# Optimization experiments

Measured on AMD Instinct MI355X. Metric: run time of the kernel, lower is better.

## Reference

```python
import jax, jax.numpy as jnp
import numpy as np

PARTITIONS = 8
TWO_PI = 2.0 * np.pi
EPS_COUNT = 0.0001  # added to bin counts to avoid div-by-zero


def setup_inputs() -> dict:
    key = jax.random.key(0)
    k1, k2, k3, k4 = jax.random.split(key, 4)
    B, N, T = 16384, 128, 8
    trajs = jax.random.normal(k1, (B, T, 2), dtype=jnp.float32)
    nei_trajs = jax.random.normal(k2, (B, N, T, 2), dtype=jnp.float32)
    # mark last 32 neighbors as invalid (all-zero trajectories -> masked out)
    nei_trajs = nei_trajs.at[:, N - 32:].set(0.0)
    # TrajEncoding: Dense(dim=3 -> output_units=128) + ReLU
    W_ce = jax.random.normal(k3, (3, 128), dtype=jnp.float32) * (1.0 / np.sqrt(3.0))
    b_ce = jnp.zeros((128,), dtype=jnp.float32)
    return {"trajs": trajs, "nei_trajs": nei_trajs, "W_ce": W_ce, "b_ce": b_ce}


def reference(trajs, nei_trajs, W_ce, b_ce):
    # trajs: [B, T, 2]; nei_trajs: [B, N, T, 2]
    nei_vector = nei_trajs[..., -1, :] - nei_trajs[..., 0, :]      # [B, N, 2]
    nei_pos = nei_trajs[..., -1, :]                                 # [B, N, 2]

    # factors (use_velocity, use_distance, use_direction; rel_velocity=False)
    f_velocity = jnp.linalg.norm(nei_vector, axis=-1)               # [B, N]
    f_distance = jnp.linalg.norm(nei_pos, axis=-1)                  # [B, N]
    f_direction = jnp.arctan2(nei_pos[..., 0], nei_pos[..., 1]) % TWO_PI  # [B, N]

    angle_idx = (f_direction / (TWO_PI / PARTITIONS)).astype(jnp.int32)   # [B, N]
    nei_mask = (jnp.sum(nei_trajs, axis=(-1, -2)) != 0).astype(jnp.int32)  # [B, N]
    angle_idx = angle_idx * nei_mask + (-1) * (1 - nei_mask)

    # one-hot over partitions replaces the python loop: [B, N, P]
    onehot = (angle_idx[..., None] == jnp.arange(PARTITIONS, dtype=jnp.int32)).astype(jnp.float32)
    n = jnp.sum(onehot, axis=1) + EPS_COUNT                         # [B, P]

    feats = jnp.stack([f_velocity, f_distance, f_direction], axis=-1)  # [B, N, 3]
    sums = jnp.einsum('bnf,bnp->bpf', feats, onehot)                # [B, P, 3]
    social_circle = sums / n[..., None]                             # [B, P, 3]

    f_sc = jax.nn.relu(social_circle @ W_ce + b_ce)                 # [B, P, 128]
    return f_sc, social_circle
```

## Files before the change

### kernel.cpp

```cpp
#include <hip/hip_runtime.h>
#include <math.h>

#define NPART 8
#define NN    128

typedef float f32x4 __attribute__((ext_vector_type(4)));

__global__ __launch_bounds__(256) void sc_kernel(
    const float* __restrict__ nei,
    const float* __restrict__ W,
    const float* __restrict__ bce,
    float* __restrict__ fsc,
    float* __restrict__ scout,
    int Btot)
{
    const int tid  = threadIdx.x;
    const int lane = tid & 63;
    const int wv   = tid >> 6;
    const int b    = blockIdx.x * 4 + wv;
    if (b >= Btot) return;

    __shared__ float s_sum[4][NPART * 3];
    __shared__ float s_cnt[4][NPART];
    __shared__ float s_sc[4][NPART * 3];

    const f32x4* src = reinterpret_cast<const f32x4*>(nei) + (size_t)b * (NN * 4);
    f32x4 a0 = __builtin_nontemporal_load(src + lane * 4 + 0);
    f32x4 c0 = __builtin_nontemporal_load(src + lane * 4 + 1);
    f32x4 d0 = __builtin_nontemporal_load(src + lane * 4 + 2);
    f32x4 e0 = __builtin_nontemporal_load(src + lane * 4 + 3);
    f32x4 a1 = __builtin_nontemporal_load(src + 256 + lane * 4 + 0);
    f32x4 c1 = __builtin_nontemporal_load(src + 256 + lane * 4 + 1);
    f32x4 d1 = __builtin_nontemporal_load(src + 256 + lane * 4 + 2);
    f32x4 e1 = __builtin_nontemporal_load(src + 256 + lane * 4 + 3);

    const int c0i = 4 * (lane & 31);
    f32x4 wr0 = *reinterpret_cast<const f32x4*>(W + 0 * NN + c0i);
    f32x4 wr1 = *reinterpret_cast<const f32x4*>(W + 1 * NN + c0i);
    f32x4 wr2 = *reinterpret_cast<const f32x4*>(W + 2 * NN + c0i);
    f32x4 bb  = *reinterpret_cast<const f32x4*>(bce + c0i);

    if (lane < NPART * 3) s_sum[wv][lane] = 0.0f;
    if (lane < NPART)     s_cnt[wv][lane] = 0.0f;
    __builtin_amdgcn_wave_barrier();

    const float TWOPI = 6.2831853071795864769f;
    const float STEP  = (float)(6.283185307179586 / 8.0);

    #pragma unroll
    for (int h = 0; h < 2; ++h) {
        f32x4 a = h ? a1 : a0;
        f32x4 c = h ? c1 : c0;
        f32x4 d = h ? d1 : d0;
        f32x4 e = h ? e1 : e0;

        float total = (((a.x + a.y) + (a.z + a.w)) + ((c.x + c.y) + (c.z + c.w)))
                    + (((d.x + d.y) + (d.z + d.w)) + ((e.x + e.y) + (e.z + e.w)));

        float px = e.z, py = e.w;
        float vx = px - a.x, vy = py - a.y;
        float fvel  = sqrtf(vx * vx + vy * vy);
        float fdist = sqrtf(px * px + py * py);

        float fdir = atan2f(px, py);
        if (fdir < 0.0f) fdir += TWOPI;

        int idx = (int)(fdir / STEP);

        if (total != 0.0f && idx >= 0 && idx < NPART) {
            atomicAdd(&s_sum[wv][idx * 3 + 0], fvel);
            atomicAdd(&s_sum[wv][idx * 3 + 1], fdist);
            atomicAdd(&s_sum[wv][idx * 3 + 2], fdir);
            atomicAdd(&s_cnt[wv][idx], 1.0f);
        }
    }
    __builtin_amdgcn_wave_barrier();

    if (lane < NPART * 3) {
        float v = s_sum[wv][lane] / (s_cnt[wv][lane / 3] + 0.0001f);
        s_sc[wv][lane] = v;
        __builtin_nontemporal_store(v, scout + (size_t)b * (NPART * 3) + lane);
    }
    __builtin_amdgcn_wave_barrier();

    float* o = fsc + (size_t)b * NPART * NN;
    #pragma unroll
    for (int s = 0; s < 4; ++s) {
        int p = 2 * s + (lane >> 5);
        float sv = s_sc[wv][p * 3 + 0];
        float sd = s_sc[wv][p * 3 + 1];
        float sr = s_sc[wv][p * 3 + 2];
        f32x4 acc;
        acc.x = fmaxf(fmaf(sv, wr0.x, fmaf(sd, wr1.x, fmaf(sr, wr2.x, bb.x))), 0.0f);
        acc.y = fmaxf(fmaf(sv, wr0.y, fmaf(sd, wr1.y, fmaf(sr, wr2.y, bb.y))), 0.0f);
        acc.z = fmaxf(fmaf(sv, wr0.z, fmaf(sd, wr1.z, fmaf(sr, wr2.z, bb.z))), 0.0f);
        acc.w = fmaxf(fmaf(sv, wr0.w, fmaf(sd, wr1.w, fmaf(sr, wr2.w, bb.w))), 0.0f);
        __builtin_nontemporal_store(acc, reinterpret_cast<f32x4*>(o + p * NN + c0i));
    }
}

extern "C" void kernel_launch(void* const* d_in, const int* in_sizes, int n_in,
                              void* d_out, int out_size, void* d_ws, size_t ws_size,
                              hipStream_t stream) {
    const float* nei = (const float*)d_in[1];
    const float* W   = (const float*)d_in[2];
    const float* bce = (const float*)d_in[3];

    const int Btot = in_sizes[1] / (NN * 8 * 2);

    float* fsc   = (float*)d_out;
    float* scout = fsc + (size_t)Btot * NPART * NN;

    const int nblk = (Btot + 3) / 4;
    sc_kernel<<<nblk, 256, 0, stream>>>(nei, W, bce, fsc, scout, Btot);
}
```

Before: 51.84 us.

## Use fast polynomial atan2, split LDS histograms per half-wave, drop nontemporal hints

Replaces the library atan2f with a custom minimax polynomial that uses hardware reciprocal and returns the angle directly in [0, 2π). The bin index is now computed by multiplying by a constant instead of dividing. The shared-memory histogram is duplicated per half-wave to cut atomic contention, and the two copies are summed at the end. Nontemporal loads and stores become plain accesses, and the weight loads move after the reduction. This adds a small accuracy risk near bin boundaries and changes how the memory streams are cached.

Measured after the change: 44.30 us. 1.17x faster.

```diff
diff --git a/kernel.cpp b/kernel.cpp
--- a/kernel.cpp
+++ b/kernel.cpp
@@ -5,6 +5,33 @@
 #define NN    128
 
 typedef float f32x4 __attribute__((ext_vector_type(4)));
+
+__device__ __forceinline__ float atan2_2pi(float y, float x) {
+    const float PI_F    = 3.14159265358979f;
+    const float PIO2_F  = 1.57079632679490f;
+    const float PIO4_F  = 0.78539816339745f;
+    const float TWOPI_F = 6.28318530717959f;
+    float ay = fabsf(y), ax = fabsf(x);
+    float mn = fminf(ay, ax), mx = fmaxf(ay, ax);
+    float r  = __builtin_amdgcn_rcpf(mx);
+    float q  = mn * r;
+    q = fmaf(fmaf(-mx, q, mn), r, q);
+    bool  big  = q > 0.41421356237f;
+    float num2 = q - 1.0f, den2 = q + 1.0f;
+    float r2   = __builtin_amdgcn_rcpf(den2);
+    float q2   = num2 * r2;
+    q2 = fmaf(fmaf(-den2, q2, num2), r2, q2);
+    float t = big ? q2 : q;
+    float u = t * t;
+    float p = fmaf(u, 8.05374449538e-2f, -1.38776856032e-1f);
+    p = fmaf(u, p, 1.99777106478e-1f);
+    p = fmaf(u, p, -3.33329491539e-1f);
+    float z0 = fmaf(p * u, t, t);
+    if (big) z0 += PIO4_F;
+    float zq = (ay > ax) ? (PIO2_F - z0) : z0;
+    float z1 = (x < 0.0f) ? (PI_F - zq) : zq;
+    return (y < 0.0f) ? (TWOPI_F - z1) : z1;
+}
 
 __global__ __launch_bounds__(256) void sc_kernel(
     const float* __restrict__ nei,
@@ -17,35 +44,30 @@
     const int tid  = threadIdx.x;
     const int lane = tid & 63;
     const int wv   = tid >> 6;
+    const int hi   = lane >> 5;
     const int b    = blockIdx.x * 4 + wv;
     if (b >= Btot) return;
 
-    __shared__ float s_sum[4][NPART * 3];
-    __shared__ float s_cnt[4][NPART];
+    __shared__ float s_sum[4][2][NPART * 3];
+    __shared__ float s_cnt[4][2][NPART];
     __shared__ float s_sc[4][NPART * 3];
 
     const f32x4* src = reinterpret_cast<const f32x4*>(nei) + (size_t)b * (NN * 4);
-    f32x4 a0 = __builtin_nontemporal_load(src + lane * 4 + 0);
-    f32x4 c0 = __builtin_nontemporal_load(src + lane * 4 + 1);
-    f32x4 d0 = __builtin_nontemporal_load(src + lane * 4 + 2);
-    f32x4 e0 = __builtin_nontemporal_load(src + lane * 4 + 3);
-    f32x4 a1 = __builtin_nontemporal_load(src + 256 + lane * 4 + 0);
-    f32x4 c1 = __builtin_nontemporal_load(src + 256 + lane * 4 + 1);
-    f32x4 d1 = __builtin_nontemporal_load(src + 256 + lane * 4 + 2);
-    f32x4 e1 = __builtin_nontemporal_load(src + 256 + lane * 4 + 3);
+    f32x4 a0 = src[lane * 4 + 0];
+    f32x4 c0 = src[lane * 4 + 1];
+    f32x4 d0 = src[lane * 4 + 2];
+    f32x4 e0 = src[lane * 4 + 3];
+    f32x4 a1 = src[256 + lane * 4 + 0];
+    f32x4 c1 = src[256 + lane * 4 + 1];
+    f32x4 d1 = src[256 + lane * 4 + 2];
+    f32x4 e1 = src[256 + lane * 4 + 3];
 
-    const int c0i = 4 * (lane & 31);
-    f32x4 wr0 = *reinterpret_cast<const f32x4*>(W + 0 * NN + c0i);
-    f32x4 wr1 = *reinterpret_cast<const f32x4*>(W + 1 * NN + c0i);
-    f32x4 wr2 = *reinterpret_cast<const f32x4*>(W + 2 * NN + c0i);
-    f32x4 bb  = *reinterpret_cast<const f32x4*>(bce + c0i);
-
-    if (lane < NPART * 3) s_sum[wv][lane] = 0.0f;
-    if (lane < NPART)     s_cnt[wv][lane] = 0.0f;
+    {
+        int ll = lane & 31;
+        if (ll < NPART * 3) s_sum[wv][hi][ll] = 0.0f;
+        else                s_cnt[wv][hi][ll - NPART * 3] = 0.0f;
+    }
     __builtin_amdgcn_wave_barrier();
-
-    const float TWOPI = 6.2831853071795864769f;
-    const float STEP  = (float)(6.283185307179586 / 8.0);
 
     #pragma unroll
     for (int h = 0; h < 2; ++h) {
@@ -62,31 +84,36 @@
         float fvel  = sqrtf(vx * vx + vy * vy);
         float fdist = sqrtf(px * px + py * py);
 
-        float fdir = atan2f(px, py);
-        if (fdir < 0.0f) fdir += TWOPI;
-
-        int idx = (int)(fdir / STEP);
+        float fdir = atan2_2pi(px, py);
+        int idx = (int)(fdir * 1.27323954474f);
 
         if (total != 0.0f && idx >= 0 && idx < NPART) {
-            atomicAdd(&s_sum[wv][idx * 3 + 0], fvel);
-            atomicAdd(&s_sum[wv][idx * 3 + 1], fdist);
-            atomicAdd(&s_sum[wv][idx * 3 + 2], fdir);
-            atomicAdd(&s_cnt[wv][idx], 1.0f);
+            atomicAdd(&s_sum[wv][hi][idx * 3 + 0], fvel);
+            atomicAdd(&s_sum[wv][hi][idx * 3 + 1], fdist);
+            atomicAdd(&s_sum[wv][hi][idx * 3 + 2], fdir);
+            atomicAdd(&s_cnt[wv][hi][idx], 1.0f);
         }
     }
     __builtin_amdgcn_wave_barrier();
 
     if (lane < NPART * 3) {
-        float v = s_sum[wv][lane] / (s_cnt[wv][lane / 3] + 0.0001f);
+        float v = (s_sum[wv][0][lane] + s_sum[wv][1][lane]) /
+                  (s_cnt[wv][0][lane / 3] + s_cnt[wv][1][lane / 3] + 0.0001f);
         s_sc[wv][lane] = v;
-        __builtin_nontemporal_store(v, scout + (size_t)b * (NPART * 3) + lane);
+        scout[(size_t)b * (NPART * 3) + lane] = v;
     }
     __builtin_amdgcn_wave_barrier();
+
+    const int c0i = 4 * (lane & 31);
+    f32x4 wr0 = *reinterpret_cast<const f32x4*>(W + 0 * NN + c0i);
+    f32x4 wr1 = *reinterpret_cast<const f32x4*>(W + 1 * NN + c0i);
+    f32x4 wr2 = *reinterpret_cast<const f32x4*>(W + 2 * NN + c0i);
+    f32x4 bb  = *reinterpret_cast<const f32x4*>(bce + c0i);
 
     float* o = fsc + (size_t)b * NPART * NN;
     #pragma unroll
     for (int s = 0; s < 4; ++s) {
-        int p = 2 * s + (lane >> 5);
+        int p = 2 * s + hi;
         float sv = s_sc[wv][p * 3 + 0];
         float sd = s_sc[wv][p * 3 + 1];
         float sr = s_sc[wv][p * 3 + 2];
@@ -95,7 +122,7 @@
         acc.y = fmaxf(fmaf(sv, wr0.y, fmaf(sd, wr1.y, fmaf(sr, wr2.y, bb.y))), 0.0f);
         acc.z = fmaxf(fmaf(sv, wr0.z, fmaf(sd, wr1.z, fmaf(sr, wr2.z, bb.z))), 0.0f);
         acc.w = fmaxf(fmaf(sv, wr0.w, fmaf(sd, wr1.w, fmaf(sr, wr2.w, bb.w))), 0.0f);
-        __builtin_nontemporal_store(acc, reinterpret_cast<f32x4*>(o + p * NN + c0i));
+        *reinterpret_cast<f32x4*>(o + p * NN + c0i) = acc;
     }
 }
 
@@ -111,6 +138,5 @@
     float* fsc   = (float*)d_out;
     float* scout = fsc + (size_t)Btot * NPART * NN;
 
-    const int nblk = (Btot + 3) / 4;
-    sc_kernel<<<nblk, 256, 0, stream>>>(nei, W, bce, fsc, scout, Btot);
+    sc_kernel<<<(Btot + 3) / 4, 256, 0, stream>>>(nei, W, bce, fsc, scout, Btot);
 }
```
